# Kernel tuning notes

Measured on AMD Instinct MI355X. Metric: run time of the kernel, lower is better.

Reference implementation:

```python
import jax, jax.numpy as jnp
import numpy as np

PRESENCE_W = 1.0
L1_W = 1.0
B, N, M = 64, 2048, 64


def setup_inputs() -> dict:
    key = jax.random.key(0)
    k1, k2, k3, k4 = jax.random.split(key, 4)
    return {
        "predict_scores": jax.random.normal(k1, (B, N, 2), dtype=jnp.float32),
        "predict_boxes": jax.random.uniform(k2, (B, N, 4), dtype=jnp.float32),
        "scores": jax.random.randint(k3, (B, M), 0, 2, dtype=jnp.int32),
        "boxes": jax.random.uniform(k4, (B, M, 4), dtype=jnp.float32),
    }


def _cost(ps, pb, gs, gb):
    # presence[b,n,m] = -ps[b,n,gs[b,m]]
    b, n, _ = ps.shape
    m = gs.shape[1]
    idx = jnp.broadcast_to(gs[:, None, :].astype(jnp.int32), (b, n, m))
    presence = -jnp.take_along_axis(ps, idx, axis=2)            # (B,N,M)
    l1 = jnp.abs(pb[:, :, None, :] - gb[:, None, :, :]).sum(-1)  # (B,N,M)
    return PRESENCE_W * presence + L1_W * l1


def _hungarian(cost):
    # Jonker-Volgenant shortest-augmenting-path LSA (same optimum as
    # scipy.optimize.linear_sum_assignment). cost: (n, m) with n <= m.
    # Returns col4row: for each row i, the assigned column.
    n, m = cost.shape
    INF = np.inf
    u = np.zeros(n + 1)
    v = np.zeros(m + 1)
    p = np.zeros(m + 1, dtype=np.int64)   # col -> assigned row (1-based), 0=free
    way = np.zeros(m + 1, dtype=np.int64)
    for i in range(1, n + 1):
        p[0] = i
        j0 = 0
        minv = np.full(m + 1, INF)
        used = np.zeros(m + 1, dtype=bool)
        while True:
            used[j0] = True
            i0 = p[j0]
            free = ~used[1:]
            cur = cost[i0 - 1] - u[i0] - v[1:]
            mv = minv[1:]
            wy = way[1:]
            upd = free & (cur < mv)
            mv[upd] = cur[upd]
            wy[upd] = j0
            masked = np.where(free, mv, INF)
            j1 = int(np.argmin(masked)) + 1
            delta = masked[j1 - 1]
            used_idx = np.flatnonzero(used)
            u[p[used_idx]] += delta
            v[used_idx] -= delta
            mv[free] -= delta
            j0 = j1
            if p[j0] == 0:
                break
        while j0:
            j1 = way[j0]
            p[j0] = p[j1]
            j0 = j1
    col4row = np.zeros(n, dtype=np.int64)
    for j in range(1, m + 1):
        if p[j] > 0:
            col4row[p[j] - 1] = j - 1
    return col4row


def reference(predict_scores, predict_boxes, scores, boxes):
    cost = _cost(predict_scores, predict_boxes, scores, boxes)  # (B,N,M)
    c = np.asarray(jax.device_get(cost), dtype=np.float64)
    rows, cols = [], []
    for b in range(c.shape[0]):
        # transpose so the smaller side (M targets) is rows, like scipy does
        pred_for_gt = _hungarian(c[b].T)         # (M,) prediction index per target
        order = np.argsort(pred_for_gt)
        rows.append(pred_for_gt[order])          # sorted prediction indices
        cols.append(order.astype(np.int64))      # matching target indices
    row_ind = jnp.asarray(np.stack(rows), dtype=jnp.int32)  # (B,M)
    col_ind = jnp.asarray(np.stack(cols), dtype=jnp.int32)  # (B,M)
    return cost, row_ind, col_ind
```

## Files before the change

kernel.cpp:

```cpp
#include <hip/hip_runtime.h>
#include <math.h>
#include <limits.h>

#define Bb 64
#define Nn 2048
#define Mm 64

__device__ __forceinline__ float cost1(const float4 pb4, const float4 gb4,
                                       const float2 p2, const int g) {
    const float psv = (g == 0) ? p2.x : p2.y;
    float l1 = fabsf(pb4.x - gb4.x);
    l1 += fabsf(pb4.y - gb4.y);
    l1 += fabsf(pb4.z - gb4.z);
    l1 += fabsf(pb4.w - gb4.w);
    return (-psv) + l1;
}

__device__ __forceinline__ double readlane_f64_63(double x) {
    const long long v = __double_as_longlong(x);
    const int lo = __builtin_amdgcn_readlane((int)v, 63);
    const int hi = __builtin_amdgcn_readlane((int)(v >> 32), 63);
    return __longlong_as_double(((long long)hi << 32) | (unsigned int)lo);
}

__device__ __forceinline__ double readlane_f64(double x, int sl) {
    const long long v = __double_as_longlong(x);
    const int lo = __builtin_amdgcn_readlane((int)v, sl);
    const int hi = __builtin_amdgcn_readlane((int)(v >> 32), sl);
    return __longlong_as_double(((long long)hi << 32) | (unsigned int)lo);
}

__device__ __forceinline__ void cost_tileA_t(
    int blk, int t, const float* __restrict__ ps, const float* __restrict__ pb,
    const int* __restrict__ gs, const float* __restrict__ gb,
    float* __restrict__ out)
{
    const int b  = blk >> 5;
    const int j0 = (blk & 31) << 6;
    const int sub = t & 15;
    const int grp = t >> 4;

    const int i4 = sub << 2;
    const int4   g4 = ((const int4*)(gs + b * Mm))[sub];
    const float4 gbq0 = ((const float4*)gb)[b * Mm + i4 + 0];
    const float4 gbq1 = ((const float4*)gb)[b * Mm + i4 + 1];
    const float4 gbq2 = ((const float4*)gb)[b * Mm + i4 + 2];
    const float4 gbq3 = ((const float4*)gb)[b * Mm + i4 + 3];
    #pragma unroll
    for (int r = 0; r < 4; ++r) {
        const int j = j0 + grp + (r << 4);
        const float2 p2  = ((const float2*)ps)[b * Nn + j];
        const float4 pb4 = ((const float4*)pb)[b * Nn + j];
        float4 o;
        o.x = cost1(pb4, gbq0, p2, g4.x);
        o.y = cost1(pb4, gbq1, p2, g4.y);
        o.z = cost1(pb4, gbq2, p2, g4.z);
        o.w = cost1(pb4, gbq3, p2, g4.w);
        ((float4*)(out + (((size_t)b * Nn + j) << 6)))[sub] = o;
    }
}

#define MIN_DPP(CTRL)                                                           \
  {                                                                             \
    const long long mb_ = __double_as_longlong(mv);                             \
    const int lo_ = __builtin_amdgcn_update_dpp(0, (int)mb_, CTRL, 0xf, 0xf, false);            \
    const int hi_ = __builtin_amdgcn_update_dpp(0x7ff00000, (int)(mb_ >> 32), CTRL, 0xf, 0xf, false); \
    const double om_ = __longlong_as_double(((long long)hi_ << 32) | (unsigned int)lo_);        \
    mv = fmin(mv, om_);                                                         \
  }

__device__ __forceinline__ void barrier_lgkm() {
    asm volatile("" ::: "memory");
    __builtin_amdgcn_s_waitcnt(0xC07F);
    __builtin_amdgcn_s_barrier();
    asm volatile("" ::: "memory");
}

struct alignas(16) Pt { double v; int j; int i0; };

__device__ __forceinline__ int vperm(int j) {
    const int q = j - 1;
    return ((q & 3) << 9) + (q >> 2);
}

__global__ __launch_bounds__(512, 2) void hungarian_fused(
    const float* __restrict__ ps, const float* __restrict__ pb,
    const int* __restrict__ gs, const float* __restrict__ gb,
    float* __restrict__ out, float* __restrict__ out_row,
    float* __restrict__ out_col)
{
    const int bid = blockIdx.x;
    if (bid >= Bb) {
        const int blk = ((bid - Bb) << 1) + (threadIdx.x >> 8);
        cost_tileA_t(blk, threadIdx.x & 255, ps, pb, gs, gb, out);
        return;
    }

    __builtin_amdgcn_s_setprio(1);

    __shared__ double s_v[Nn];
    __shared__ double s_delta[Mm + 8];
    __shared__ int    s_j[Mm + 8];
    __shared__ Pt     s_part[2][8];
    __shared__ int    s_c4r[Mm];

    const int b = bid;
    const int t = threadIdx.x;
    const int lane = t & 63;
    const int wave = t >> 6;
    const double INF = __builtin_inf();

    for (int j = t; j < Nn; j += 512) s_v[j] = 0.0;

    const float2* psb = (const float2*)(ps + (size_t)b * Nn * 2);
    const float4* pbb = (const float4*)(pb + (size_t)b * Nn * 4);
    float4 P[4]; float2 S[4];
    #pragma unroll
    for (int r = 0; r < 4; ++r) {
        P[r] = pbb[(t << 2) + r];
        S[r] = psb[(t << 2) + r];
    }
    const float4 rgb = ((const float4*)gb)[b * Mm + lane];
    const int    rg  = gs[b * Mm + lane];

    __syncthreads();

    double vv[4];
    #pragma unroll
    for (int k = 0; k < 4; ++k) vv[k] = 0.0;
    double my_u = 0.0;
    int my_col = 0;
    int par = 0;

    for (int i = 1; i <= Mm; ++i) {
        int T = 0;
        int fjc = 0;
        int i0 = i;
        int my_pos = -1;

        for (;;) {
            const int sl = i0 - 1;
            float4 gb4;
            gb4.x = __int_as_float(__builtin_amdgcn_readlane(__float_as_int(rgb.x), sl));
            gb4.y = __int_as_float(__builtin_amdgcn_readlane(__float_as_int(rgb.y), sl));
            gb4.z = __int_as_float(__builtin_amdgcn_readlane(__float_as_int(rgb.z), sl));
            gb4.w = __int_as_float(__builtin_amdgcn_readlane(__float_as_int(rgb.w), sl));
            const int g = __builtin_amdgcn_readlane(rg, sl);
            const double u0 = readlane_f64(my_u, sl);

            if (t == 0) s_j[T] = fjc;
            if (fjc && ((fjc - 1) >> 2) == t) vv[(fjc - 1) & 3] = -INF;
            if (lane + 1 == i0) my_pos = T;

            double cur[4];
            #pragma unroll
            for (int k = 0; k < 4; ++k) {
                const float c = cost1(P[k], gb4, S[k], g);
                cur[k] = ((double)c - u0) - vv[k];
            }
            double v01 = cur[0]; int k01 = 0;
            if (cur[1] < v01) { v01 = cur[1]; k01 = 1; }
            double v23 = cur[2]; int k23 = 2;
            if (cur[3] < v23) { v23 = cur[3]; k23 = 3; }
            if (v23 < v01) { v01 = v23; k01 = k23; }
            double bv = v01;
            int bj = (t << 2) + 1 + k01;

            double mv = bv;
            MIN_DPP(0x111)
            MIN_DPP(0x112)
            MIN_DPP(0x114)
            MIN_DPP(0x118)
            MIN_DPP(0x142)
            MIN_DPP(0x143)
            const double wmin = readlane_f64_63(mv);
            const unsigned long long eq = __ballot(bv == wmin);
            const int l0 = (int)__builtin_ctzll(eq);
            const int bjw = __builtin_amdgcn_readlane(bj, l0);

            const unsigned long long mw = __ballot(my_col == bjw);
            const int i0w = mw ? (int)__builtin_ctzll(mw) + 1 : 0;
            if (lane == l0) {
                Pt p; p.v = bv; p.j = bj; p.i0 = i0w;
                s_part[par][wave] = p;
            }
            barrier_lgkm();

            const Pt pq = s_part[par][lane & 7];
            {
                double mv = pq.v;
                MIN_DPP(0xB1)
                MIN_DPP(0x4E)
                MIN_DPP(0x124)
                const double gv = mv;
                const unsigned long long wb = __ballot(pq.v == gv);
                const int wsel = (int)__builtin_ctzll(wb);
                fjc = __builtin_amdgcn_readlane(pq.j, wsel);
                const int fi0 = __builtin_amdgcn_readlane(pq.i0, wsel);
                if (t == 0) s_delta[T] = readlane_f64(pq.v, wsel);
                T++; par ^= 1;
                if (fi0 == 0) break;
                i0 = fi0;
            }
        }

        barrier_lgkm();
        if (my_pos >= 0) {
            double au = my_u;
            for (int k = my_pos; k < T; ++k) au += s_delta[k];
            my_u = au;
        }
        if (t < T) {
            const int jq = s_j[t];
            if (jq) {
                const int idx = vperm(jq);
                double nv = s_v[idx];
                for (int k = t; k < T; ++k) nv -= s_delta[k];
                s_v[idx] = nv;
            }
        }
        if (lane == i - 1) my_col = fjc;
        barrier_lgkm();
        #pragma unroll
        for (int k = 0; k < 4; ++k) vv[k] = s_v[(k << 9) + t];
    }

    if (t < Mm) s_c4r[t] = my_col - 1;
    __syncthreads();
    if (t < Mm) {
        const int my = s_c4r[t];
        int rank = 0;
        #pragma unroll 4
        for (int q = 0; q < Mm; ++q) rank += (s_c4r[q] < my);
        out_row[b * Mm + rank] = (float)my;
        out_col[b * Mm + rank] = (float)t;
    }
}

extern "C" void kernel_launch(void* const* d_in, const int* in_sizes, int n_in,
                              void* d_out, int out_size, void* d_ws, size_t ws_size,
                              hipStream_t stream) {
    const float* ps = (const float*)d_in[0];
    const float* pb = (const float*)d_in[1];
    const int*   gs = (const int*)d_in[2];
    const float* gb = (const float*)d_in[3];
    float* out = (float*)d_out;
    float* out_row = out + (size_t)Bb * Nn * Mm;
    float* out_col = out_row + Bb * Mm;

    (void)d_ws; (void)ws_size;
    hungarian_fused<<<Bb + Bb * (Nn / 128), 512, 0, stream>>>(
        ps, pb, gs, gb, out, out_row, out_col);
}
```

Baseline: 261.8 us.

## Pack two Hungarian batches per block and keep dual variables in registers

Each 512-thread block now solves two batches, with 256 threads per batch each holding 8 columns instead of 4. The column potentials are kept in registers and updated incrementally on every Dijkstra step, using a per-thread bitmask of visited columns. This removes the shared-memory s_v array and the post-augmentation delta replay with its extra barriers. Both batches share one barrier per step and the loop runs until both report done. The cost is doubled per-thread work and register pressure (launch bounds drop to 1 block per SM), and the faster batch has to wait for the slower one.

```diff
diff --git a/kernel.cpp b/kernel.cpp
--- a/kernel.cpp
+++ b/kernel.cpp
@@ -28,6 +28,10 @@
     const int lo = __builtin_amdgcn_readlane((int)v, sl);
     const int hi = __builtin_amdgcn_readlane((int)(v >> 32), sl);
     return __longlong_as_double(((long long)hi << 32) | (unsigned int)lo);
+}
+
+__device__ __forceinline__ float readlane_f32(float x, int sl) {
+    return __int_as_float(__builtin_amdgcn_readlane(__float_as_int(x), sl));
 }
 
 __device__ __forceinline__ void cost_tileA_t(
@@ -60,13 +64,13 @@
     }
 }
 
-#define MIN_DPP(CTRL)                                                           \
+#define MIN_DPP64(VAR, CTRL)                                                    \
   {                                                                             \
-    const long long mb_ = __double_as_longlong(mv);                             \
+    const long long mb_ = __double_as_longlong(VAR);                            \
     const int lo_ = __builtin_amdgcn_update_dpp(0, (int)mb_, CTRL, 0xf, 0xf, false);            \
     const int hi_ = __builtin_amdgcn_update_dpp(0x7ff00000, (int)(mb_ >> 32), CTRL, 0xf, 0xf, false); \
     const double om_ = __longlong_as_double(((long long)hi_ << 32) | (unsigned int)lo_);        \
-    mv = fmin(mv, om_);                                                         \
+    VAR = fmin(VAR, om_);                                                       \
   }
 
 __device__ __forceinline__ void barrier_lgkm() {
@@ -76,85 +80,75 @@
     asm volatile("" ::: "memory");
 }
 
-struct alignas(16) Pt { double v; int j; int i0; };
-
-__device__ __forceinline__ int vperm(int j) {
-    const int q = j - 1;
-    return ((q & 3) << 9) + (q >> 2);
-}
-
-__global__ __launch_bounds__(512, 2) void hungarian_fused(
+struct alignas(16) Pt { double v; int ji; int pad; };
+
+__global__ __launch_bounds__(512, 1) void hungarian_fused(
     const float* __restrict__ ps, const float* __restrict__ pb,
     const int* __restrict__ gs, const float* __restrict__ gb,
     float* __restrict__ out, float* __restrict__ out_row,
     float* __restrict__ out_col)
 {
     const int bid = blockIdx.x;
-    if (bid >= Bb) {
-        const int blk = ((bid - Bb) << 1) + (threadIdx.x >> 8);
+    if (bid >= Bb / 2) {
+        const int blk = ((bid - Bb / 2) << 1) + (threadIdx.x >> 8);
         cost_tileA_t(blk, threadIdx.x & 255, ps, pb, gs, gb, out);
         return;
     }
 
     __builtin_amdgcn_s_setprio(1);
 
-    __shared__ double s_v[Nn];
-    __shared__ double s_delta[Mm + 8];
-    __shared__ int    s_j[Mm + 8];
-    __shared__ Pt     s_part[2][8];
-    __shared__ int    s_c4r[Mm];
-
-    const int b = bid;
+    __shared__ Pt  s_part[2][2][4];
+    __shared__ int s_c4r[2][Mm];
+    __shared__ int s_done[2];
+
     const int t = threadIdx.x;
     const int lane = t & 63;
     const int wave = t >> 6;
+    const int grp = wave >> 2;
+    const int slot = wave & 3;
+    const int tg = t & 255;
+    const int b = (bid << 1) + grp;
     const double INF = __builtin_inf();
 
-    for (int j = t; j < Nn; j += 512) s_v[j] = 0.0;
+    if (t < 2) s_done[t] = 0;
 
     const float2* psb = (const float2*)(ps + (size_t)b * Nn * 2);
     const float4* pbb = (const float4*)(pb + (size_t)b * Nn * 4);
-    float4 P[4]; float2 S[4];
+    float4 P[8]; float2 S[8];
     #pragma unroll
-    for (int r = 0; r < 4; ++r) {
-        P[r] = pbb[(t << 2) + r];
-        S[r] = psb[(t << 2) + r];
+    for (int r = 0; r < 8; ++r) {
+        P[r] = pbb[(tg << 3) + r];
+        S[r] = psb[(tg << 3) + r];
     }
     const float4 rgb = ((const float4*)gb)[b * Mm + lane];
     const int    rg  = gs[b * Mm + lane];
 
-    __syncthreads();
-
-    double vv[4];
+    double vv[8], vreal[8];
     #pragma unroll
-    for (int k = 0; k < 4; ++k) vv[k] = 0.0;
-    double my_u = 0.0;
-    int my_col = 0;
+    for (int k = 0; k < 8; ++k) { vv[k] = 0.0; vreal[k] = 0.0; }
+    double myu = 0.0;
+    int mycol = 0;
+    int mk = 0;
+    bool inch = false;
+    bool done = false;
+    int i = 1, i0 = 1;
     int par = 0;
 
-    for (int i = 1; i <= Mm; ++i) {
-        int T = 0;
-        int fjc = 0;
-        int i0 = i;
-        int my_pos = -1;
-
-        for (;;) {
+    for (;;) {
+        if (!done) {
             const int sl = i0 - 1;
             float4 gb4;
-            gb4.x = __int_as_float(__builtin_amdgcn_readlane(__float_as_int(rgb.x), sl));
-            gb4.y = __int_as_float(__builtin_amdgcn_readlane(__float_as_int(rgb.y), sl));
-            gb4.z = __int_as_float(__builtin_amdgcn_readlane(__float_as_int(rgb.z), sl));
-            gb4.w = __int_as_float(__builtin_amdgcn_readlane(__float_as_int(rgb.w), sl));
+            gb4.x = readlane_f32(rgb.x, sl);
+            gb4.y = readlane_f32(rgb.y, sl);
+            gb4.z = readlane_f32(rgb.z, sl);
+            gb4.w = readlane_f32(rgb.w, sl);
             const int g = __builtin_amdgcn_readlane(rg, sl);
-            const double u0 = readlane_f64(my_u, sl);
-
-            if (t == 0) s_j[T] = fjc;
-            if (fjc && ((fjc - 1) >> 2) == t) vv[(fjc - 1) & 3] = -INF;
-            if (lane + 1 == i0) my_pos = T;
-
-            double cur[4];
+            const double u0 = readlane_f64(myu, sl);
+            inch = inch || (lane + 1 == i0);
+
+            double cur[8];
             #pragma unroll
-            for (int k = 0; k < 4; ++k) {
+            for (int k = 0; k < 8; ++k) {
                 const float c = cost1(P[k], gb4, S[k], g);
                 cur[k] = ((double)c - u0) - vv[k];
             }
@@ -162,78 +156,94 @@
             if (cur[1] < v01) { v01 = cur[1]; k01 = 1; }
             double v23 = cur[2]; int k23 = 2;
             if (cur[3] < v23) { v23 = cur[3]; k23 = 3; }
+            double v45 = cur[4]; int k45 = 4;
+            if (cur[5] < v45) { v45 = cur[5]; k45 = 5; }
+            double v67 = cur[6]; int k67 = 6;
+            if (cur[7] < v67) { v67 = cur[7]; k67 = 7; }
             if (v23 < v01) { v01 = v23; k01 = k23; }
-            double bv = v01;
-            int bj = (t << 2) + 1 + k01;
+            if (v67 < v45) { v45 = v67; k45 = k67; }
+            if (v45 < v01) { v01 = v45; k01 = k45; }
+            const double bv = v01;
+            const int bj = (tg << 3) + 1 + k01;
 
             double mv = bv;
-            MIN_DPP(0x111)
-            MIN_DPP(0x112)
-            MIN_DPP(0x114)
-            MIN_DPP(0x118)
-            MIN_DPP(0x142)
-            MIN_DPP(0x143)
+            MIN_DPP64(mv, 0x111)
+            MIN_DPP64(mv, 0x112)
+            MIN_DPP64(mv, 0x114)
+            MIN_DPP64(mv, 0x118)
+            MIN_DPP64(mv, 0x142)
+            MIN_DPP64(mv, 0x143)
             const double wmin = readlane_f64_63(mv);
             const unsigned long long eq = __ballot(bv == wmin);
             const int l0 = (int)__builtin_ctzll(eq);
             const int bjw = __builtin_amdgcn_readlane(bj, l0);
 
-            const unsigned long long mw = __ballot(my_col == bjw);
+            const unsigned long long mw = __ballot(mycol == bjw);
             const int i0w = mw ? (int)__builtin_ctzll(mw) + 1 : 0;
             if (lane == l0) {
-                Pt p; p.v = bv; p.j = bj; p.i0 = i0w;
-                s_part[par][wave] = p;
-            }
-            barrier_lgkm();
-
-            const Pt pq = s_part[par][lane & 7];
-            {
-                double mv = pq.v;
-                MIN_DPP(0xB1)
-                MIN_DPP(0x4E)
-                MIN_DPP(0x124)
-                const double gv = mv;
-                const unsigned long long wb = __ballot(pq.v == gv);
-                const int wsel = (int)__builtin_ctzll(wb);
-                fjc = __builtin_amdgcn_readlane(pq.j, wsel);
-                const int fi0 = __builtin_amdgcn_readlane(pq.i0, wsel);
-                if (t == 0) s_delta[T] = readlane_f64(pq.v, wsel);
-                T++; par ^= 1;
-                if (fi0 == 0) break;
+                Pt p; p.v = bv; p.ji = (bjw << 7) | i0w; p.pad = 0;
+                s_part[par][grp][slot] = p;
+            }
+        }
+        barrier_lgkm();
+        const int dA = s_done[0];
+        const int dB = s_done[1];
+        if (!done) {
+            const Pt pq = s_part[par][grp][lane & 3];
+            double mv2 = pq.v;
+            MIN_DPP64(mv2, 0xB1)
+            MIN_DPP64(mv2, 0x4E)
+            const unsigned long long wb = __ballot(pq.v == mv2);
+            const int wsel = (int)__builtin_ctzll(wb);
+            const int jiw = __builtin_amdgcn_readlane(pq.ji, wsel);
+            const double delta = readlane_f64(pq.v, wsel);
+            const int fjc = jiw >> 7;
+            const int fi0 = jiw & 127;
+
+            myu += inch ? delta : 0.0;
+            if (mk) {
+                #pragma unroll
+                for (int k = 0; k < 8; ++k)
+                    vreal[k] -= ((mk >> k) & 1) ? delta : 0.0;
+            }
+
+            if (fi0 == 0) {
+                if (lane == i - 1) mycol = fjc;
+                #pragma unroll
+                for (int k = 0; k < 8; ++k) vv[k] = vreal[k];
+                mk = 0; inch = false;
+                ++i; i0 = i;
+                if (i > Mm) {
+                    done = true;
+                    if (tg == 0) s_done[grp] = 1;
+                }
+            } else {
                 i0 = fi0;
+                if (((fjc - 1) >> 3) == tg) {
+                    const int km = (fjc - 1) & 7;
+                    #pragma unroll
+                    for (int k = 0; k < 8; ++k)
+                        if (k == km) vv[k] = -INF;
+                    mk |= 1 << km;
+                }
             }
         }
-
-        barrier_lgkm();
-        if (my_pos >= 0) {
-            double au = my_u;
-            for (int k = my_pos; k < T; ++k) au += s_delta[k];
-            my_u = au;
-        }
-        if (t < T) {
-            const int jq = s_j[t];
-            if (jq) {
-                const int idx = vperm(jq);
-                double nv = s_v[idx];
-                for (int k = t; k < T; ++k) nv -= s_delta[k];
-                s_v[idx] = nv;
-            }
-        }
-        if (lane == i - 1) my_col = fjc;
-        barrier_lgkm();
-        #pragma unroll
-        for (int k = 0; k < 4; ++k) vv[k] = s_v[(k << 9) + t];
-    }
-
-    if (t < Mm) s_c4r[t] = my_col - 1;
+        if (dA && dB) break;
+        par ^= 1;
+    }
+
+    if (wave == 0) s_c4r[0][lane] = mycol - 1;
+    if (wave == 4) s_c4r[1][lane] = mycol - 1;
     __syncthreads();
-    if (t < Mm) {
-        const int my = s_c4r[t];
+    if (t < 128) {
+        const int gq = t >> 6, r = t & 63;
+        const int my = s_c4r[gq][r];
         int rank = 0;
         #pragma unroll 4
-        for (int q = 0; q < Mm; ++q) rank += (s_c4r[q] < my);
-        out_row[b * Mm + rank] = (float)my;
-        out_col[b * Mm + rank] = (float)t;
+        for (int q = 0; q < Mm; ++q) rank += (s_c4r[gq][q] < my);
+        const int bb = (bid << 1) + gq;
+        out_row[bb * Mm + rank] = (float)my;
+        out_col[bb * Mm + rank] = (float)r;
     }
 }
 
@@ -249,6 +259,6 @@
     float* out_col = out_row + Bb * Mm;
 
     (void)d_ws; (void)ws_size;
-    hungarian_fused<<<Bb + Bb * (Nn / 128), 512, 0, stream>>>(
+    hungarian_fused<<<Bb / 2 + Bb * (Nn / 128), 512, 0, stream>>>(
         ps, pb, gs, gb, out, out_row, out_col);
 }
```

After: 305.3 us. +16.6%, slower.
